# Kernel optimization log

Hardware: AMD Instinct MI355X
Metric: run time of the kernel (lower is better)

## Reference

```python
import jax, jax.numpy as jnp
import numpy as np

ANCHORS = np.array([[30.0, 61.0], [62.0, 45.0], [59.0, 119.0]], dtype=np.float32)
STRIDE = 16.0
NUM_CLASSES = 80
NB, NH, NW, NT = 16, 64, 64, 50
IGNORE_THRESH = 0.5


def _iou_cxcywh(b1, b2):
    # b1, b2: broadcastable (..., 4) boxes in (cx, cy, w, h); faithful to multi_bbox_ious(x1y1x2y2=False)
    x1, y1, w1, h1 = b1[..., 0], b1[..., 1], b1[..., 2], b1[..., 3]
    x2, y2, w2, h2 = b2[..., 0], b2[..., 1], b2[..., 2], b2[..., 3]
    mx = jnp.minimum(x1 - w1 * 0.5, x2 - w2 * 0.5)
    Mx = jnp.maximum(x1 + w1 * 0.5, x2 + w2 * 0.5)
    my = jnp.minimum(y1 - h1 * 0.5, y2 - h2 * 0.5)
    My = jnp.maximum(y1 + h1 * 0.5, y2 + h2 * 0.5)
    cw = w1 + w2 - (Mx - mx)
    ch = h1 + h2 - (My - my)
    carea = jnp.where((cw <= 0) | (ch <= 0), 0.0, cw * ch)
    uarea = w1 * h1 + w2 * h2 - carea
    return carea / uarea


def _build_targets(pred_boxes, target, anchors, nH, nW):
    nB = target.shape[0]
    nA = anchors.shape[0]
    nT = target.shape[1] // 5
    nAnchors = nA * nH * nW
    pb = pred_boxes.reshape(nB, nAnchors, 4)
    tbox = target.reshape(nB, nT, 5)
    # torch loop breaks at first target with x == 0 -> prefix validity mask
    valid = jnp.cumprod((tbox[:, :, 1] != 0).astype(jnp.int32), axis=1) > 0
    gx = tbox[:, :, 1] * nW
    gy = tbox[:, :, 2] * nH
    gw = tbox[:, :, 3] * nW
    gh = tbox[:, :, 4] * nH
    gt = jnp.stack([gx, gy, gw, gh], axis=-1)                    # (nB, nT, 4)
    ious = _iou_cxcywh(pb[:, None, :, :], gt[:, :, None, :])     # (nB, nT, nAnchors)
    cur_ious = jnp.max(jnp.where(valid[:, :, None], ious, 0.0), axis=1)
    conf_mask = jnp.where(cur_ious > IGNORE_THRESH, 0.0, 1.0).reshape(nB, nA, nH, nW)
    # best anchor per gt: IoU between zero-centered gt and zero-centered anchors
    anc0 = jnp.concatenate([jnp.zeros_like(anchors), anchors], axis=1)      # (nA, 4)
    gt0 = jnp.concatenate([jnp.zeros_like(gt[..., :2]), gt[..., 2:]], -1)   # (nB, nT, 4)
    a_ious = _iou_cxcywh(gt0[:, :, None, :], anc0[None, None, :, :])        # (nB, nT, nA)
    best_n = jnp.argmax(a_ious, axis=2)  # first-max, matches torch.max tie-break
    gi = jnp.clip(jnp.floor(gx).astype(jnp.int32), 0, nW - 1)
    gj = jnp.clip(jnp.floor(gy).astype(jnp.int32), 0, nH - 1)
    tx = gx - gi.astype(gx.dtype)
    ty = gy - gj.astype(gy.dtype)
    tw = jnp.log(gw / anchors[best_n, 0])
    th = jnp.log(gh / anchors[best_n, 1])
    tc = tbox[:, :, 0]
    coord_mask = jnp.zeros((nB, nA, nH, nW), jnp.float32)
    cls_mask = jnp.zeros((nB, nA, nH, nW), jnp.float32)
    tconf = jnp.zeros((nB, nA, nH, nW), jnp.float32)
    tcls = jnp.zeros((nB, nA, nH, nW), jnp.float32)
    tcoord = jnp.zeros((4, nB, nA, nH, nW), jnp.float32)
    bidx = jnp.arange(nB)

    def step(carry, xs):
        coord_mask, conf_mask, cls_mask, tcoord, tconf, tcls = carry
        bn, gj_t, gi_t, v, txv, tyv, twv, thv, tcv = xs  # each (nB,)

        def upd(arr, val):
            cur = arr[bidx, bn, gj_t, gi_t]
            return arr.at[bidx, bn, gj_t, gi_t].set(jnp.where(v, val, cur))

        coord_mask = upd(coord_mask, 1.0)
        cls_mask = upd(cls_mask, 1.0)
        conf_mask = upd(conf_mask, 1.0)
        tconf = upd(tconf, 1.0)
        tcls = upd(tcls, tcv)
        vals = jnp.stack([txv, tyv, twv, thv])            # (4, nB)
        cur = tcoord[:, bidx, bn, gj_t, gi_t]
        tcoord = tcoord.at[:, bidx, bn, gj_t, gi_t].set(jnp.where(v[None, :], vals, cur))
        return (coord_mask, conf_mask, cls_mask, tcoord, tconf, tcls), None

    xs = tuple(a.T for a in (best_n, gj, gi, valid, tx, ty, tw, th, tc))  # scan over targets, sequential overwrite order as in torch
    (coord_mask, conf_mask, cls_mask, tcoord, tconf, tcls), _ = jax.lax.scan(
        step, (coord_mask, conf_mask, cls_mask, tcoord, tconf, tcls), xs)
    return coord_mask, conf_mask, cls_mask, tcoord, tconf, tcls


def _yolo_loss(output, target):
    anchors = jnp.asarray(ANCHORS / STRIDE)
    nB, nA, nC = output.shape[0], ANCHORS.shape[0], NUM_CLASSES
    nH, nW = output.shape[2], output.shape[3]
    cad = nB * nA * nH * nW
    out5 = output.reshape(nB, nA, 5 + nC, nH, nW)
    coord_raw = jnp.transpose(out5[:, :, 0:4], (2, 0, 1, 3, 4)).reshape(4, cad)
    coord = jnp.concatenate([jax.nn.sigmoid(coord_raw[0:2]), coord_raw[2:4]], axis=0)
    conf = jax.nn.sigmoid(out5[:, :, 4])                         # (nB, nA, nH, nW)
    grid_x = jnp.broadcast_to(jnp.arange(nW, dtype=jnp.float32), (nB * nA, nH, nW)).reshape(-1)
    grid_y = jnp.broadcast_to(jnp.arange(nH, dtype=jnp.float32)[:, None], (nB * nA, nH, nW)).reshape(-1)
    # NOTE: anchor-major flattening replicated faithfully from the torch source (repeat(1, nB*nH*nW))
    anchor_w = jnp.broadcast_to(anchors[:, 0:1], (nA, nB * nH * nW)).reshape(-1)
    anchor_h = jnp.broadcast_to(anchors[:, 1:2], (nA, nB * nH * nW)).reshape(-1)
    pred_boxes = jnp.stack([coord[0] + grid_x, coord[1] + grid_y,
                            jnp.exp(coord[2]) * anchor_w, jnp.exp(coord[3]) * anchor_h], axis=1)
    tgt = jax.lax.stop_gradient(target)  # torch: target.detach()
    masks = _build_targets(jax.lax.stop_gradient(pred_boxes), tgt, anchors, nH, nW)
    coord_mask, conf_mask, cls_mask, tcoord, tconf, tcls = jax.tree_util.tree_map(jax.lax.stop_gradient, masks)
    cm = coord_mask.reshape(cad)
    tcoord_f = tcoord.reshape(4, cad)
    loss_coord = 0.5 * jnp.sum((coord * cm - tcoord_f * cm) ** 2)
    loss_conf = jnp.sum((conf * conf_mask - tconf * conf_mask) ** 2)
    cls = jnp.transpose(out5[:, :, 5:], (0, 1, 3, 4, 2)).reshape(cad, nC)
    logp = jax.nn.log_softmax(cls, axis=-1)
    tcls_i = tcls.reshape(cad).astype(jnp.int32)
    picked = jnp.take_along_axis(logp, tcls_i[:, None], axis=1)[:, 0]
    loss_cls = -jnp.sum(cls_mask.reshape(cad) * picked)
    return loss_coord + loss_conf + loss_cls


def setup_inputs() -> dict:
    key = jax.random.key(0)
    k_out, kc, kx, ky, kw, kh = jax.random.split(key, 6)
    output = jax.random.normal(k_out, (NB, 3 * (5 + NUM_CLASSES), NH, NW), dtype=jnp.float32)
    cls_id = jnp.floor(jax.random.uniform(kc, (NB, NT)) * NUM_CLASSES)
    cx = jax.random.uniform(kx, (NB, NT), minval=0.02, maxval=0.98)
    cy = jax.random.uniform(ky, (NB, NT), minval=0.02, maxval=0.98)
    bw = jax.random.uniform(kw, (NB, NT), minval=0.05, maxval=0.5)
    bh = jax.random.uniform(kh, (NB, NT), minval=0.05, maxval=0.5)
    target = jnp.stack([cls_id, cx, cy, bw, bh], axis=-1).reshape(NB, NT * 5).astype(jnp.float32)
    return {"output": output, "target": target}


def reference(output, target):
    return _yolo_loss(output, target)
```

## Files before the change

### kernel.cpp

```cpp
#include <hip/hip_runtime.h>
#include <math.h>

#define NBATCH 16
#define NANCH  3
#define NHH    64
#define NWW    64
#define NTT    50
#define NCLS   80
#define HW     (NHH*NWW)
#define CELLS  (NBATCH*NANCH*HW)
#define CELLBLOCKS (CELLS/256)
#define TPB    13
#define TBLOCKS (NBATCH*TPB)

#define AW0 1.875f
#define AW1 3.875f
#define AW2 3.6875f
#define AH0 3.8125f
#define AH1 2.8125f
#define AH2 7.4375f

__device__ __forceinline__ void prep_targets(const float* __restrict__ target, int b, int tid,
                                             float* s_gx, float* s_gy, float* s_gw, float* s_gh,
                                             float* s_xlo, float* s_xhi, float* s_ylo, float* s_yhi,
                                             float* s_area, int* s_meta) {
    const float* tb0 = target + b * (NTT * 5);
    float c1 = 0.f, c2 = 0.f, c3 = 0.f, c4 = 0.f;
    bool nz = false;
    if (tid < NTT) {
        c1 = tb0[tid * 5 + 1]; c2 = tb0[tid * 5 + 2];
        c3 = tb0[tid * 5 + 3]; c4 = tb0[tid * 5 + 4];
        nz = (c1 != 0.0f);
    }
    const unsigned long long mask = __ballot(nz);
    const int first_zero = __ffsll((unsigned long long)~mask) - 1;
    if (tid < NTT) {
        const bool valid = tid < first_zero;
        const float gx = c1 * NWW, gy = c2 * NHH;
        const float gw = c3 * NWW, gh = c4 * NHH;

        const float ga = gw * gh;
        const float i0 = fminf(gw, AW0) * fminf(gh, AH0);
        const float i1 = fminf(gw, AW1) * fminf(gh, AH1);
        const float i2 = fminf(gw, AW2) * fminf(gh, AH2);
        const float r0 = i0 / (ga + AW0 * AH0 - i0);
        const float r1 = i1 / (ga + AW1 * AH1 - i1);
        const float r2 = i2 / (ga + AW2 * AH2 - i2);
        int best = 0; float bv = r0;
        if (r1 > bv) { bv = r1; best = 1; }
        if (r2 > bv) { bv = r2; best = 2; }

        int gi = (int)floorf(gx); gi = gi < 0 ? 0 : (gi > NWW - 1 ? NWW - 1 : gi);
        int gj = (int)floorf(gy); gj = gj < 0 ? 0 : (gj > NHH - 1 ? NHH - 1 : gj);

        s_gx[tid] = gx; s_gy[tid] = gy; s_gw[tid] = gw; s_gh[tid] = gh;
        s_xlo[tid] = gx - gw * 0.5f; s_xhi[tid] = gx + gw * 0.5f;
        s_ylo[tid] = gy - gh * 0.5f; s_yhi[tid] = gy + gh * 0.5f;
        s_area[tid] = ga;
        s_meta[tid] = valid ? ((1 << 15) | (best << 12) | (gj << 6) | gi) : 0;
    }
}

__global__ __launch_bounds__(256) void yolo_loss_kernel(
    const float* __restrict__ out,
    const float* __restrict__ target,
    float* __restrict__ loss)
{
    __shared__ float s_gx[NTT], s_gy[NTT], s_gw[NTT], s_gh[NTT];
    __shared__ float s_xlo[NTT], s_xhi[NTT], s_ylo[NTT], s_yhi[NTT], s_area[NTT];
    __shared__ int   s_meta[NTT];
    __shared__ float s_part[4];

    const int tid  = threadIdx.x;
    const int lane = tid & 63, wid = tid >> 6;

    if (blockIdx.x < TBLOCKS) {
        const int tb = blockIdx.x;
        const int b  = tb / TPB;
        const int t  = (tb % TPB) * 4 + wid;

        if (tid < 64)
            prep_targets(target, b, tid, s_gx, s_gy, s_gw, s_gh,
                         s_xlo, s_xhi, s_ylo, s_yhi, s_area, s_meta);
        __syncthreads();

        if (t < NTT) {
            const int m = s_meta[t];
            if (m != 0) {
                const int mv_lane = (lane < NTT) ? s_meta[lane] : 0;
                const unsigned long long dup = __ballot(lane > t && mv_lane == m);
                if (dup == 0ULL) {
                    const int best = (m >> 12) & 3;
                    const int hw   = m & 0xFFF;
                    const float* cb = out + ((size_t)(b * NANCH + best) * (5 + NCLS) + 5) * HW + hw;

                    const float l0 = cb[lane * HW];
                    const float l1 = (lane < NCLS - 64) ? cb[(lane + 64) * HW] : -INFINITY;

                    float mx = fmaxf(l0, l1);
                    #pragma unroll
                    for (int off = 32; off > 0; off >>= 1)
                        mx = fmaxf(mx, __shfl_xor(mx, off, 64));

                    float e = __expf(l0 - mx) + ((lane < NCLS - 64) ? __expf(l1 - mx) : 0.0f);
                    #pragma unroll
                    for (int off = 32; off > 0; off >>= 1)
                        e += __shfl_xor(e, off, 64);

                    if (lane == 0) {
                        const int tc = (int)target[b * (NTT * 5) + t * 5];
                        const float lt = cb[tc * HW];
                        atomicAdd(loss, -(lt - mx - __logf(e)));
                    }
                }
            }
        }
        return;
    }

    const int cblk = blockIdx.x - TBLOCKS;
    const int b    = cblk / 48;

    const int cell = cblk * 256 + tid;
    const int rem  = cell % (NANCH * HW);
    const int a    = rem / HW;
    const int hw   = rem % HW;
    const int h    = hw >> 6;
    const int w    = hw & 63;

    const float* base = out + ((size_t)b * (NANCH * (5 + NCLS)) + (size_t)a * (5 + NCLS)) * HW + hw;
    const float r0 = base[0];
    const float r1 = base[HW];
    const float r2 = base[2 * HW];
    const float r3 = base[3 * HW];
    const float r4 = base[4 * HW];

    if (tid < 64)
        prep_targets(target, b, tid, s_gx, s_gy, s_gw, s_gh,
                     s_xlo, s_xhi, s_ylo, s_yhi, s_area, s_meta);
    __syncthreads();

    const float sx = __builtin_amdgcn_rcpf(1.0f + __expf(-r0));
    const float sy = __builtin_amdgcn_rcpf(1.0f + __expf(-r1));

    const int aidx = (3 * b + a) >> 4;
    const float aw = aidx == 0 ? AW0 : (aidx == 1 ? AW1 : AW2);
    const float ah = aidx == 0 ? AH0 : (aidx == 1 ? AH1 : AH2);

    const float px = sx + (float)w;
    const float py = sy + (float)h;
    const float pw = __expf(r2) * aw;
    const float ph = __expf(r3) * ah;
    const float parea = pw * ph;

    const float hx0 = px - pw * 0.5f, hx1 = px + pw * 0.5f;
    const float hy0 = py - ph * 0.5f, hy1 = py + ph * 0.5f;

    const int key = (1 << 15) | (a << 12) | (h << 6) | w;

    float curmax = 0.0f;
    int   tlast  = -1;
    #pragma unroll 5
    for (int t = 0; t < NTT; ++t) {
        const int   m   = s_meta[t];
        const float xlo = s_xlo[t], xhi = s_xhi[t];
        const float ylo = s_ylo[t], yhi = s_yhi[t];
        const float ga  = s_area[t];
        const float mx = fminf(hx0, xlo), Mx = fmaxf(hx1, xhi);
        const float my = fminf(hy0, ylo), My = fmaxf(hy1, yhi);
        const float cw = (pw + (xhi - xlo)) - (Mx - mx);
        const float ch = (ph + (yhi - ylo)) - (My - my);
        const float carea = (cw <= 0.0f || ch <= 0.0f) ? 0.0f : cw * ch;
        const float uarea = parea + ga - carea;
        const float iou   = carea * __builtin_amdgcn_rcpf(uarea);
        curmax = fmaxf(curmax, (m != 0) ? iou : 0.0f);
        if (m == key) tlast = t;
    }

    const float conf = __builtin_amdgcn_rcpf(1.0f + __expf(-r4));
    float lsum;
    if (tlast >= 0) {
        const int best = (s_meta[tlast] >> 12) & 3;
        const float baw = best == 0 ? AW0 : (best == 1 ? AW1 : AW2);
        const float bah = best == 0 ? AH0 : (best == 1 ? AH1 : AH2);
        const float tx = s_gx[tlast] - (float)w;
        const float ty = s_gy[tlast] - (float)h;
        const float tw = __logf(s_gw[tlast] * __builtin_amdgcn_rcpf(baw));
        const float th = __logf(s_gh[tlast] * __builtin_amdgcn_rcpf(bah));

        const float dx = sx - tx, dy = sy - ty, dw = r2 - tw, dh = r3 - th;
        const float dc = conf - 1.0f;
        lsum = dc * dc + 0.5f * (dx * dx + dy * dy + dw * dw + dh * dh);
    } else {
        lsum = (curmax > 0.5f) ? 0.0f : conf * conf;
    }

    float v = lsum;
    #pragma unroll
    for (int off = 32; off > 0; off >>= 1) v += __shfl_down(v, off, 64);
    if (lane == 0) s_part[wid] = v;
    __syncthreads();
    if (tid == 0)
        atomicAdd(loss, s_part[0] + s_part[1] + s_part[2] + s_part[3]);
}

extern "C" void kernel_launch(void* const* d_in, const int* in_sizes, int n_in,
                              void* d_out, int out_size, void* d_ws, size_t ws_size,
                              hipStream_t stream) {
    const float* out_t  = (const float*)d_in[0];
    const float* target = (const float*)d_in[1];
    float* loss = (float*)d_out;

    hipMemsetAsync(loss, 0, sizeof(float), stream);
    yolo_loss_kernel<<<TBLOCKS + CELLBLOCKS, 256, 0, stream>>>(out_t, target, loss);
}
```

Before: 107.5 us.

## Replace global atomics with per-block partials and a reduce kernel; pack target boxes

Measured after the change: 96.13 us. 10.6% less time.

```diff
diff --git a/kernel.cpp b/kernel.cpp
--- a/kernel.cpp
+++ b/kernel.cpp
@@ -12,6 +12,7 @@
 #define CELLBLOCKS (CELLS/256)
 #define TPB    13
 #define TBLOCKS (NBATCH*TPB)
+#define NPART  (TBLOCKS + CELLBLOCKS)
 
 #define AW0 1.875f
 #define AW1 3.875f
@@ -22,8 +23,7 @@
 
 __device__ __forceinline__ void prep_targets(const float* __restrict__ target, int b, int tid,
                                              float* s_gx, float* s_gy, float* s_gw, float* s_gh,
-                                             float* s_xlo, float* s_xhi, float* s_ylo, float* s_yhi,
-                                             float* s_area, int* s_meta) {
+                                             float4* s_box, float2* s_gam, int* s_meta) {
     const float* tb0 = target + b * (NTT * 5);
     float c1 = 0.f, c2 = 0.f, c3 = 0.f, c4 = 0.f;
     bool nz = false;
@@ -53,23 +53,25 @@
         int gi = (int)floorf(gx); gi = gi < 0 ? 0 : (gi > NWW - 1 ? NWW - 1 : gi);
         int gj = (int)floorf(gy); gj = gj < 0 ? 0 : (gj > NHH - 1 ? NHH - 1 : gj);
 
+        const int m = valid ? ((1 << 15) | (best << 12) | (gj << 6) | gi) : 0;
         s_gx[tid] = gx; s_gy[tid] = gy; s_gw[tid] = gw; s_gh[tid] = gh;
-        s_xlo[tid] = gx - gw * 0.5f; s_xhi[tid] = gx + gw * 0.5f;
-        s_ylo[tid] = gy - gh * 0.5f; s_yhi[tid] = gy + gh * 0.5f;
-        s_area[tid] = ga;
-        s_meta[tid] = valid ? ((1 << 15) | (best << 12) | (gj << 6) | gi) : 0;
+        s_box[tid] = make_float4(gx - gw * 0.5f, gx + gw * 0.5f,
+                                 gy - gh * 0.5f, gy + gh * 0.5f);
+        s_gam[tid] = make_float2(ga, __int_as_float(m));
+        s_meta[tid] = m;
     }
 }
 
 __global__ __launch_bounds__(256) void yolo_loss_kernel(
     const float* __restrict__ out,
     const float* __restrict__ target,
-    float* __restrict__ loss)
+    float* __restrict__ partials)
 {
-    __shared__ float s_gx[NTT], s_gy[NTT], s_gw[NTT], s_gh[NTT];
-    __shared__ float s_xlo[NTT], s_xhi[NTT], s_ylo[NTT], s_yhi[NTT], s_area[NTT];
-    __shared__ int   s_meta[NTT];
-    __shared__ float s_part[4];
+    __shared__ float  s_gx[NTT], s_gy[NTT], s_gw[NTT], s_gh[NTT];
+    __shared__ float4 s_box[NTT];
+    __shared__ float2 s_gam[NTT];
+    __shared__ int    s_meta[NTT];
+    __shared__ float  s_part[4];
 
     const int tid  = threadIdx.x;
     const int lane = tid & 63, wid = tid >> 6;
@@ -80,10 +82,10 @@
         const int t  = (tb % TPB) * 4 + wid;
 
         if (tid < 64)
-            prep_targets(target, b, tid, s_gx, s_gy, s_gw, s_gh,
-                         s_xlo, s_xhi, s_ylo, s_yhi, s_area, s_meta);
+            prep_targets(target, b, tid, s_gx, s_gy, s_gw, s_gh, s_box, s_gam, s_meta);
         __syncthreads();
 
+        float nll = 0.0f;
         if (t < NTT) {
             const int m = s_meta[t];
             if (m != 0) {
@@ -110,11 +112,15 @@
                     if (lane == 0) {
                         const int tc = (int)target[b * (NTT * 5) + t * 5];
                         const float lt = cb[tc * HW];
-                        atomicAdd(loss, -(lt - mx - __logf(e)));
+                        nll = -(lt - mx - __logf(e));
                     }
                 }
             }
         }
+        if (lane == 0) s_part[wid] = nll;
+        __syncthreads();
+        if (tid == 0)
+            partials[blockIdx.x] = s_part[0] + s_part[1] + s_part[2] + s_part[3];
         return;
     }
 
@@ -136,8 +142,7 @@
     const float r4 = base[4 * HW];
 
     if (tid < 64)
-        prep_targets(target, b, tid, s_gx, s_gy, s_gw, s_gh,
-                     s_xlo, s_xhi, s_ylo, s_yhi, s_area, s_meta);
+        prep_targets(target, b, tid, s_gx, s_gy, s_gw, s_gh, s_box, s_gam, s_meta);
     __syncthreads();
 
     const float sx = __builtin_amdgcn_rcpf(1.0f + __expf(-r0));
@@ -162,16 +167,13 @@
     int   tlast  = -1;
     #pragma unroll 5
     for (int t = 0; t < NTT; ++t) {
-        const int   m   = s_meta[t];
-        const float xlo = s_xlo[t], xhi = s_xhi[t];
-        const float ylo = s_ylo[t], yhi = s_yhi[t];
-        const float ga  = s_area[t];
-        const float mx = fminf(hx0, xlo), Mx = fmaxf(hx1, xhi);
-        const float my = fminf(hy0, ylo), My = fmaxf(hy1, yhi);
-        const float cw = (pw + (xhi - xlo)) - (Mx - mx);
-        const float ch = (ph + (yhi - ylo)) - (My - my);
+        const float4 bx  = s_box[t];
+        const float2 gam = s_gam[t];
+        const int    m   = __float_as_int(gam.y);
+        const float cw = fminf(hx1, bx.y) - fmaxf(hx0, bx.x);
+        const float ch = fminf(hy1, bx.w) - fmaxf(hy0, bx.z);
         const float carea = (cw <= 0.0f || ch <= 0.0f) ? 0.0f : cw * ch;
-        const float uarea = parea + ga - carea;
+        const float uarea = parea + gam.x - carea;
         const float iou   = carea * __builtin_amdgcn_rcpf(uarea);
         curmax = fmaxf(curmax, (m != 0) ? iou : 0.0f);
         if (m == key) tlast = t;
@@ -201,7 +203,22 @@
     if (lane == 0) s_part[wid] = v;
     __syncthreads();
     if (tid == 0)
-        atomicAdd(loss, s_part[0] + s_part[1] + s_part[2] + s_part[3]);
+        partials[blockIdx.x] = s_part[0] + s_part[1] + s_part[2] + s_part[3];
+}
+
+__global__ __launch_bounds__(256) void yolo_reduce_kernel(
+    const float* __restrict__ partials, float* __restrict__ loss)
+{
+    __shared__ float s_part[4];
+    const int tid = threadIdx.x;
+    float v = 0.0f;
+    for (int i = tid; i < NPART; i += 256) v += partials[i];
+    #pragma unroll
+    for (int off = 32; off > 0; off >>= 1) v += __shfl_down(v, off, 64);
+    const int lane = tid & 63, wid = tid >> 6;
+    if (lane == 0) s_part[wid] = v;
+    __syncthreads();
+    if (tid == 0) loss[0] = s_part[0] + s_part[1] + s_part[2] + s_part[3];
 }
 
 extern "C" void kernel_launch(void* const* d_in, const int* in_sizes, int n_in,
@@ -209,8 +226,9 @@
                               hipStream_t stream) {
     const float* out_t  = (const float*)d_in[0];
     const float* target = (const float*)d_in[1];
-    float* loss = (float*)d_out;
-
-    hipMemsetAsync(loss, 0, sizeof(float), stream);
-    yolo_loss_kernel<<<TBLOCKS + CELLBLOCKS, 256, 0, stream>>>(out_t, target, loss);
-}
+    float* loss     = (float*)d_out;
+    float* partials = (float*)d_ws;
+
+    yolo_loss_kernel<<<NPART, 256, 0, stream>>>(out_t, target, partials);
+    yolo_reduce_kernel<<<1, 256, 0, stream>>>(partials, loss);
+}
```
